# Optimization experiments

Hardware: AMD Instinct MI355X
Metric: run time of the kernel (lower is better)

## Reference

```python
import jax, jax.numpy as jnp
import numpy as np

N_NODES = 50000
N_EDGES = 800000
IN_FEATS = 128
HIDDEN = 128
OUT_LEN = 128


def setup_inputs() -> dict:
    key = jax.random.key(0)
    ks = jax.random.split(key, 8)
    feat = jax.random.normal(ks[0], (N_NODES, IN_FEATS), dtype=jnp.float32)
    # Glorot-ish init for weights, zeros for bias (DGL GraphConv default)
    def w(k, fi, fo):
        return jax.random.normal(k, (fi, fo), dtype=jnp.float32) / np.sqrt(fi)
    W1 = w(ks[1], IN_FEATS, HIDDEN)
    W2 = w(ks[2], HIDDEN, HIDDEN)
    W3 = w(ks[3], HIDDEN, OUT_LEN)
    b1 = jnp.zeros((HIDDEN,), jnp.float32)
    b2 = jnp.zeros((HIDDEN,), jnp.float32)
    b3 = jnp.zeros((OUT_LEN,), jnp.float32)
    src = jax.random.randint(ks[4], (N_EDGES,), 0, N_NODES, dtype=jnp.int32)
    dst = jax.random.randint(ks[5], (N_EDGES,), 0, N_NODES, dtype=jnp.int32)
    return {"feat": feat, "W1": W1, "b1": b1, "W2": W2, "b2": b2,
            "W3": W3, "b3": b3, "src": src, "dst": dst}


def _degree_norm(idx, n):
    # degree counts, clamped to min 1 (DGL behavior), then ^{-1/2}
    deg = jax.ops.segment_sum(jnp.ones_like(idx, dtype=jnp.float32), idx,
                              num_segments=n)
    return jax.lax.rsqrt(jnp.maximum(deg, 1.0))


def _graph_conv(x, W, b, src, dst, out_norm, in_norm):
    # DGL GraphConv, norm='both':
    # h = D_dst^{-1/2} * segsum_dst( D_src^{-1/2} * x[src] ) @ W + b
    h = x * out_norm[:, None]
    m = jax.ops.segment_sum(h[src], dst, num_segments=x.shape[0])  # [N, d]
    m = m * in_norm[:, None]
    return m @ W + b


def reference(feat, W1, b1, W2, b2, W3, b3, src, dst):
    out_norm = _degree_norm(src, feat.shape[0])  # out-degree norm (source)
    in_norm = _degree_norm(dst, feat.shape[0])   # in-degree norm (dest)
    h = jax.nn.relu(_graph_conv(feat, W1, b1, src, dst, out_norm, in_norm))
    h = jax.nn.relu(_graph_conv(h, W2, b2, src, dst, out_norm, in_norm))
    h = _graph_conv(h, W3, b3, src, dst, out_norm, in_norm)
    # single graph: mean_nodes == mean over all nodes, then squeeze -> [out_len]
    return jnp.mean(h, axis=0)
```

## Files before the change

kernel.cpp:

```cpp
#include <hip/hip_runtime.h>

#define N_NODES 50000
#define N_EDGES 800000
#define F 128
#define SCAN_NB 49
#define CH 64
#define EPC (N_EDGES / CH)
#define HALF 25000
#define QTR 12500
#define BSTRIDE 17
#define AGG_NB (N_NODES / 4)
#define RED_NB 256

typedef __bf16 bf16x8 __attribute__((ext_vector_type(8)));
typedef float  f32x4  __attribute__((ext_vector_type(4)));
typedef float  f32x2  __attribute__((ext_vector_type(2)));

__device__ inline unsigned short f2bf(float f) {
    unsigned u = __float_as_uint(f);
    u += 0x7FFF + ((u >> 16) & 1);
    return (unsigned short)(u >> 16);
}
__device__ inline unsigned packbf2(float a, float b) {
    return (unsigned)f2bf(a) | ((unsigned)f2bf(b) << 16);
}

__device__ inline void fp8x8_to_f32(uint2 u, float* f) {
    f32x2 v0 = __builtin_amdgcn_cvt_pk_f32_fp8(u.x, false);
    f32x2 v1 = __builtin_amdgcn_cvt_pk_f32_fp8(u.x, true);
    f32x2 v2 = __builtin_amdgcn_cvt_pk_f32_fp8(u.y, false);
    f32x2 v3 = __builtin_amdgcn_cvt_pk_f32_fp8(u.y, true);
    f[0] = v0.x; f[1] = v0.y; f[2] = v1.x; f[3] = v1.y;
    f[4] = v2.x; f[5] = v2.y; f[6] = v3.x; f[7] = v3.y;
}
__device__ inline unsigned f32x4_to_fp8(float a, float b, float c, float d) {
    unsigned r = __builtin_amdgcn_cvt_pk_fp8_f32(a, b, 0, false);
    r = __builtin_amdgcn_cvt_pk_fp8_f32(c, d, r, true);
    return r;
}

__global__ __launch_bounds__(1024) void hist_kernel(const int* __restrict__ src,
                                                    const int* __restrict__ dst,
                                                    int* __restrict__ Hs,
                                                    int* __restrict__ Hd) {
    __shared__ unsigned hist[HALF / 2];
    int bx = blockIdx.x;
    int c = bx >> 2, t = bx & 1, h = (bx >> 1) & 1;
    const int* ids = t ? dst : src;
    int* H = t ? Hd : Hs;
    int base = h * HALF;
    for (int j = threadIdx.x; j < HALF / 2; j += 1024) hist[j] = 0;
    __syncthreads();
    int e0 = c * EPC;
    for (int e = e0 + threadIdx.x; e < e0 + EPC; e += 1024) {
        int id = ids[e] - base;
        if ((unsigned)id < (unsigned)HALF)
            atomicAdd(&hist[id >> 1], 1u << ((id & 1) * 16));
    }
    __syncthreads();
    for (int j = threadIdx.x; j < HALF / 2; j += 1024) {
        unsigned u = hist[j];
        uint2 o; o.x = u & 0xFFFFu; o.y = u >> 16;
        *(uint2*)&H[(size_t)c * N_NODES + base + 2 * j] = o;
    }
}

__global__ __launch_bounds__(1024) void reduceN_kernel(const int* __restrict__ Hs,
                                                       const int* __restrict__ Hd,
                                                       float* __restrict__ onorm,
                                                       float* __restrict__ inorm,
                                                       int* __restrict__ degd,
                                                       int* __restrict__ bsums) {
    __shared__ int wsum[16];
    int i = blockIdx.x * 1024 + threadIdx.x;
    int dd = 0;
    if (i < N_NODES) {
        int ds = 0;
        for (int c = 0; c < CH; c++) {
            ds += Hs[(size_t)c * N_NODES + i];
            dd += Hd[(size_t)c * N_NODES + i];
        }
        onorm[i] = rsqrtf(fmaxf((float)ds, 1.0f));
        inorm[i] = rsqrtf(fmaxf((float)dd, 1.0f));
        degd[i] = dd;
    }
    int v = dd;
#pragma unroll
    for (int off = 32; off; off >>= 1) v += __shfl_down(v, off);
    if ((threadIdx.x & 63) == 0) wsum[threadIdx.x >> 6] = v;
    __syncthreads();
    if (threadIdx.x == 0) {
        int s = 0;
#pragma unroll
        for (int k = 0; k < 16; k++) s += wsum[k];
        bsums[blockIdx.x] = s;
    }
}

__global__ __launch_bounds__(64) void scanB_kernel(const int* __restrict__ blockSums,
                                                   int* __restrict__ blockOffs) {
    int t = threadIdx.x;
    int v = (t < SCAN_NB) ? blockSums[t] : 0;
    int incl = v;
#pragma unroll
    for (int off = 1; off < 64; off <<= 1) {
        int u = __shfl_up(incl, off);
        if (t >= off) incl += u;
    }
    if (t < SCAN_NB) blockOffs[t] = incl - v;
}

__global__ __launch_bounds__(1024) void scanC_kernel(const int* __restrict__ deg,
                                                     const int* __restrict__ blockOffs,
                                                     int* __restrict__ rowst,
                                                     int* __restrict__ Hd) {
    __shared__ int wsum[16];
    int t = threadIdx.x, lane = t & 63, w = t >> 6;
    int i = blockIdx.x * 1024 + t;
    int v = (i < N_NODES) ? deg[i] : 0;
    int incl = v;
#pragma unroll
    for (int off = 1; off < 64; off <<= 1) {
        int u = __shfl_up(incl, off);
        if (lane >= off) incl += u;
    }
    if (lane == 63) wsum[w] = incl;
    __syncthreads();
    if (t == 0) {
        int s = 0;
#pragma unroll
        for (int k = 0; k < 16; k++) { int x = wsum[k]; wsum[k] = s; s += x; }
    }
    __syncthreads();
    incl += wsum[w] + blockOffs[blockIdx.x];
    if (i < N_NODES) {
        int s = incl - v;
        rowst[i] = s;
        if (i == N_NODES - 1) rowst[N_NODES] = incl;
        for (int c = 0; c < CH; c++) {
            size_t o = (size_t)c * N_NODES + i;
            int x = Hd[o]; Hd[o] = s; s += x;
        }
    }
}

__global__ __launch_bounds__(1024) void scatter2_kernel(const int* __restrict__ src,
                                                        const int* __restrict__ dst,
                                                        const float* __restrict__ onorm,
                                                        const int* __restrict__ P,
                                                        int2* __restrict__ epack) {
    __shared__ int cur[QTR];
    int bx = blockIdx.x;
    int c = bx >> 2, q = bx & 3;
    int base = q * QTR;
    for (int j = threadIdx.x; j < QTR; j += 1024)
        cur[j] = P[(size_t)c * N_NODES + base + j];
    __syncthreads();
    int e0 = c * EPC;
    for (int e = e0 + threadIdx.x; e < e0 + EPC; e += 1024) {
        int d = dst[e] - base;
        if ((unsigned)d < (unsigned)QTR) {
            int s = src[e];
            int pos = atomicAdd(&cur[d], 1);
            int2 p; p.x = s; p.y = __float_as_int(onorm[s]);
            epack[pos] = p;
        }
    }
}

__global__ __launch_bounds__(256) void cvt_kernel(const float* __restrict__ x,
                                                  uint2* __restrict__ xq, int n8) {
    int i = blockIdx.x * 256 + threadIdx.x;
    if (i < n8) {
        const float4* xv = (const float4*)x;
        float4 v0 = xv[i * 2], v1 = xv[i * 2 + 1];
        uint2 o;
        o.x = f32x4_to_fp8(v0.x, v0.y, v0.z, v0.w);
        o.y = f32x4_to_fp8(v1.x, v1.y, v1.z, v1.w);
        xq[i] = o;
    }
}

__global__ __launch_bounds__(128) void wprep_kernel(const float* __restrict__ W1,
                                                    const float* __restrict__ W2,
                                                    unsigned short* __restrict__ Wt_hi,
                                                    unsigned short* __restrict__ Wt_lo) {
    int bx = blockIdx.x;
    int wi = bx >> 7, n = bx & 127;
    const float* W = wi ? W2 : W1;
    int k = threadIdx.x;
    float v = W[k * F + n];
    unsigned short hi = f2bf(v);
    float r = v - __uint_as_float((unsigned)hi << 16);
    size_t o = (size_t)wi * F * F + (size_t)n * F + k;
    Wt_hi[o] = hi;
    Wt_lo[o] = f2bf(r);
}

template <int L3>
__global__ __launch_bounds__(256) void agg_csr_kernel(const uint2* __restrict__ xq,
                                                      uint4* __restrict__ mb,
                                                      float* __restrict__ part,
                                                      const int* __restrict__ rowst,
                                                      const int2* __restrict__ epack,
                                                      const float* __restrict__ inorm) {
    __shared__ float sP[4][F];
    int w = threadIdx.x >> 6;
    int lane = threadIdx.x & 63;
    int g = lane >> 4, t = lane & 15;
    int row = blockIdx.x * 4 + w;
    int beg = __builtin_amdgcn_readfirstlane(rowst[row]);
    int end = __builtin_amdgcn_readfirstlane(rowst[row + 1]);
    float acc[8];
#pragma unroll
    for (int k = 0; k < 8; k++) acc[k] = 0.0f;

    for (int e = beg; e < end; e += 16) {
        int ea = min(e + g,      end - 1);
        int eb = min(e + 4 + g,  end - 1);
        int ec = min(e + 8 + g,  end - 1);
        int ed = min(e + 12 + g, end - 1);
        int2 pa = epack[ea], pb = epack[eb], pc = epack[ec], pd = epack[ed];
        uint2 ua = xq[(size_t)pa.x * 16 + t];
        uint2 ub = xq[(size_t)pb.x * 16 + t];
        uint2 uc = xq[(size_t)pc.x * 16 + t];
        uint2 ud = xq[(size_t)pd.x * 16 + t];
        float wa = (e + g      < end) ? __int_as_float(pa.y) : 0.0f;
        float wb = (e + 4 + g  < end) ? __int_as_float(pb.y) : 0.0f;
        float wc = (e + 8 + g  < end) ? __int_as_float(pc.y) : 0.0f;
        float wd = (e + 12 + g < end) ? __int_as_float(pd.y) : 0.0f;
        float fa[8], fb[8], fc[8], fd[8];
        fp8x8_to_f32(ua, fa); fp8x8_to_f32(ub, fb);
        fp8x8_to_f32(uc, fc); fp8x8_to_f32(ud, fd);
#pragma unroll
        for (int k = 0; k < 8; k++)
            acc[k] += fa[k] * wa + fb[k] * wb + fc[k] * wc + fd[k] * wd;
    }
#pragma unroll
    for (int k = 0; k < 8; k++) {
        acc[k] += __shfl_xor(acc[k], 16, 64);
        acc[k] += __shfl_xor(acc[k], 32, 64);
    }
    float inw = inorm[row];
    if (!L3) {
        if (g == 0) {
            uint4 o;
            o.x = packbf2(acc[0] * inw, acc[1] * inw);
            o.y = packbf2(acc[2] * inw, acc[3] * inw);
            o.z = packbf2(acc[4] * inw, acc[5] * inw);
            o.w = packbf2(acc[6] * inw, acc[7] * inw);
            mb[(size_t)row * 16 + t] = o;
        }
    } else {
        if (g == 0) {
#pragma unroll
            for (int k = 0; k < 8; k++) sP[w][t * 8 + k] = acc[k] * inw;
        }
        __syncthreads();
        int tid = threadIdx.x;
        if (tid < F)
            part[(size_t)blockIdx.x * F + tid] =
                sP[0][tid] + sP[1][tid] + sP[2][tid] + sP[3][tid];
    }
}

__global__ __launch_bounds__(256) void mfma_gemm_kernel(const unsigned short* __restrict__ A,
                                                        const unsigned short* __restrict__ Wt_hi,
                                                        const unsigned short* __restrict__ Wt_lo,
                                                        const float* __restrict__ bias,
                                                        unsigned char* __restrict__ Y8) {
    __shared__ uint4 sB[F * BSTRIDE];
    int tid = threadIdx.x;
    int w = tid >> 6;
    int lane = tid & 63;
    int quad = lane >> 4, r16 = lane & 15;
    int row0 = blockIdx.x * 64 + w * 16;

    const uint4* Arow = (const uint4*)(A + (size_t)(row0 + r16) * F);
    uint4 a[4];
#pragma unroll
    for (int kk = 0; kk < 4; kk++) a[kk] = Arow[kk * 4 + quad];

    f32x4 acc[8];
#pragma unroll
    for (int t = 0; t < 8; t++) acc[t] = (f32x4){0.f, 0.f, 0.f, 0.f};

    const uint4* G[2] = {(const uint4*)Wt_hi, (const uint4*)Wt_lo};
#pragma unroll
    for (int ph = 0; ph < 2; ph++) {
        if (ph) __syncthreads();
        for (int j = tid; j < F * 16; j += 256)
            sB[(j >> 4) * BSTRIDE + (j & 15)] = G[ph][j];
        __syncthreads();
#pragma unroll
        for (int kk = 0; kk < 4; kk++) {
            bf16x8 av = __builtin_bit_cast(bf16x8, a[kk]);
#pragma unroll
            for (int t = 0; t < 8; t++) {
                bf16x8 bv = __builtin_bit_cast(bf16x8,
                    sB[(t * 16 + r16) * BSTRIDE + kk * 4 + quad]);
                acc[t] = __builtin_amdgcn_mfma_f32_16x16x32_bf16(av, bv, acc[t], 0, 0, 0);
            }
        }
    }

#pragma unroll
    for (int t = 0; t < 8; t++) {
        int col = t * 16 + r16;
        float bb = bias[col];
#pragma unroll
        for (int reg = 0; reg < 4; reg++) {
            int row = row0 + quad * 4 + reg;
            if (row < N_NODES) {
                float v = fmaxf(acc[t][reg] + bb, 0.0f);
                unsigned p = __builtin_amdgcn_cvt_pk_fp8_f32(v, v, 0, false);
                Y8[(size_t)row * F + col] = (unsigned char)(p & 0xFF);
            }
        }
    }
}

__global__ __launch_bounds__(128) void redpart_kernel(const float* __restrict__ part,
                                                      float* __restrict__ part2) {
    int tid = threadIdx.x;
    float acc = 0.0f;
    for (int r = blockIdx.x; r < AGG_NB; r += RED_NB)
        acc += part[(size_t)r * F + tid];
    part2[(size_t)blockIdx.x * F + tid] = acc;
}

__global__ __launch_bounds__(1024) void final_kernel(const float* __restrict__ part2,
                                                     const float* __restrict__ W3,
                                                     const float* __restrict__ b3,
                                                     float* __restrict__ out) {
    __shared__ float sc[8][F];
    int tid = threadIdx.x;
    int col = tid & 127, sl = tid >> 7;
    float acc = 0.0f;
    for (int b = sl; b < RED_NB; b += 8) acc += part2[(size_t)b * F + col];
    sc[sl][col] = acc;
    __syncthreads();
    if (tid < F) {
        float s = 0.0f;
#pragma unroll
        for (int k = 0; k < 8; k++) s += sc[k][tid];
        sc[0][tid] = s * (1.0f / (float)N_NODES);
    }
    __syncthreads();
    if (tid < F) {
        float o = b3[tid];
        for (int k = 0; k < F; k++) o += sc[0][k] * W3[k * F + tid];
        out[tid] = o;
    }
}

extern "C" void kernel_launch(void* const* d_in, const int* in_sizes, int n_in,
                              void* d_out, int out_size, void* d_ws, size_t ws_size,
                              hipStream_t stream) {
    const float* feat = (const float*)d_in[0];
    const float* W1   = (const float*)d_in[1];
    const float* b1   = (const float*)d_in[2];
    const float* W2   = (const float*)d_in[3];
    const float* b2   = (const float*)d_in[4];
    const float* W3   = (const float*)d_in[5];
    const float* b3   = (const float*)d_in[6];
    const int*   src  = (const int*)d_in[7];
    const int*   dst  = (const int*)d_in[8];
    float* out = (float*)d_out;

    char* ws = (char*)d_ws;
    size_t off = 0;
    int*   Hs    = (int*)  (ws + off);
    uint4* mb    = (uint4*)(ws + off); off += (size_t)CH * N_NODES * 4;
    int*   Hd    = (int*)  (ws + off);
    float* part  = (float*)(ws + off); off += (size_t)CH * N_NODES * 4;
    uint2* xq    = (uint2*)(ws + off); off += (size_t)N_NODES * F;
    uint2* hq    = (uint2*)(ws + off); off += (size_t)N_NODES * F;
    float* onorm = (float*)(ws + off); off += N_NODES * 4;
    float* inorm = (float*)(ws + off); off += N_NODES * 4;
    int*   rowst = (int*)  (ws + off); off += (N_NODES + 1) * 4;
    int*   bsums = (int*)  (ws + off); off += 64 * 4;
    int*   boffs = (int*)  (ws + off); off += 64 * 4;
    int*   degd  = (int*)  (ws + off); off += N_NODES * 4;
    unsigned short* Wt_hi = (unsigned short*)(ws + off); off += 2 * F * F * 2;
    unsigned short* Wt_lo = (unsigned short*)(ws + off); off += 2 * F * F * 2;
    float* part2 = (float*)(ws + off); off += (size_t)RED_NB * F * 4;
    int2*  epack = (int2*) (ws + off); off += (size_t)N_EDGES * 8;

    const int GB = (N_NODES + 63) / 64;

    hist_kernel<<<4 * CH, 1024, 0, stream>>>(src, dst, Hs, Hd);
    reduceN_kernel<<<SCAN_NB, 1024, 0, stream>>>(Hs, Hd, onorm, inorm, degd, bsums);
    scanB_kernel<<<1, 64, 0, stream>>>(bsums, boffs);
    scanC_kernel<<<SCAN_NB, 1024, 0, stream>>>(degd, boffs, rowst, Hd);
    scatter2_kernel<<<4 * CH, 1024, 0, stream>>>(src, dst, onorm, Hd, epack);

    cvt_kernel<<<(N_NODES * F / 8 + 255) / 256, 256, 0, stream>>>(feat, xq, N_NODES * F / 8);
    wprep_kernel<<<256, 128, 0, stream>>>(W1, W2, Wt_hi, Wt_lo);

    agg_csr_kernel<0><<<AGG_NB, 256, 0, stream>>>(xq, mb, part, rowst, epack, inorm);
    mfma_gemm_kernel<<<GB, 256, 0, stream>>>((const unsigned short*)mb, Wt_hi, Wt_lo, b1,
                                             (unsigned char*)hq);
    agg_csr_kernel<0><<<AGG_NB, 256, 0, stream>>>(hq, mb, part, rowst, epack, inorm);
    mfma_gemm_kernel<<<GB, 256, 0, stream>>>((const unsigned short*)mb, Wt_hi + F * F,
                                             Wt_lo + F * F, b2, (unsigned char*)xq);
    agg_csr_kernel<1><<<AGG_NB, 256, 0, stream>>>(xq, mb, part, rowst, epack, inorm);
    redpart_kernel<<<RED_NB, 128, 0, stream>>>(part, part2);
    final_kernel<<<1, 1024, 0, stream>>>(part2, W3, b3, out);
}
```

Measured before the change: 259.6 us.

## Replace third-layer aggregation with weighted column sum and fold source norm into features

The last layer's sum over destination nodes of the aggregated messages is rewritten algebraically: each source node's contribution is weighted by q[s] = sum of inorm[dst] over its out-edges, computed once by a new tq_kernel. That replaces the third full edge-gather aggregation with a single weighted column sum over nodes. The source out-degree norm is now applied when features are quantised (cvt and GEMM epilogue), so the edge list stores only 4-byte source ids instead of 8-byte id/weight pairs. Histograms move to 16-bit counts to cut workspace traffic. The cost is an extra atomic pass over the edges for q and changed rounding, since scaling now happens before fp8 quantisation.

Measured after the change: 245.9 us. 5.3% less time.

```diff
diff --git a/kernel.cpp b/kernel.cpp
--- a/kernel.cpp
+++ b/kernel.cpp
@@ -41,13 +41,13 @@
 
 __global__ __launch_bounds__(1024) void hist_kernel(const int* __restrict__ src,
                                                     const int* __restrict__ dst,
-                                                    int* __restrict__ Hs,
-                                                    int* __restrict__ Hd) {
+                                                    unsigned short* __restrict__ Hs16,
+                                                    unsigned short* __restrict__ Hd16) {
     __shared__ unsigned hist[HALF / 2];
     int bx = blockIdx.x;
     int c = bx >> 2, t = bx & 1, h = (bx >> 1) & 1;
     const int* ids = t ? dst : src;
-    int* H = t ? Hd : Hs;
+    unsigned short* H = t ? Hd16 : Hs16;
     int base = h * HALF;
     for (int j = threadIdx.x; j < HALF / 2; j += 1024) hist[j] = 0;
     __syncthreads();
@@ -58,15 +58,12 @@
             atomicAdd(&hist[id >> 1], 1u << ((id & 1) * 16));
     }
     __syncthreads();
-    for (int j = threadIdx.x; j < HALF / 2; j += 1024) {
-        unsigned u = hist[j];
-        uint2 o; o.x = u & 0xFFFFu; o.y = u >> 16;
-        *(uint2*)&H[(size_t)c * N_NODES + base + 2 * j] = o;
-    }
-}
-
-__global__ __launch_bounds__(1024) void reduceN_kernel(const int* __restrict__ Hs,
-                                                       const int* __restrict__ Hd,
+    for (int j = threadIdx.x; j < HALF / 2; j += 1024)
+        *(unsigned*)&H[(size_t)c * N_NODES + base + 2 * j] = hist[j];
+}
+
+__global__ __launch_bounds__(1024) void reduceN_kernel(const unsigned short* __restrict__ Hs16,
+                                                       const unsigned short* __restrict__ Hd16,
                                                        float* __restrict__ onorm,
                                                        float* __restrict__ inorm,
                                                        int* __restrict__ degd,
@@ -77,8 +74,8 @@
     if (i < N_NODES) {
         int ds = 0;
         for (int c = 0; c < CH; c++) {
-            ds += Hs[(size_t)c * N_NODES + i];
-            dd += Hd[(size_t)c * N_NODES + i];
+            ds += Hs16[(size_t)c * N_NODES + i];
+            dd += Hd16[(size_t)c * N_NODES + i];
         }
         onorm[i] = rsqrtf(fmaxf((float)ds, 1.0f));
         inorm[i] = rsqrtf(fmaxf((float)dd, 1.0f));
@@ -110,10 +107,34 @@
     if (t < SCAN_NB) blockOffs[t] = incl - v;
 }
 
+__global__ __launch_bounds__(1024) void tq_kernel(const int* __restrict__ src,
+                                                  const int* __restrict__ dst,
+                                                  const float* __restrict__ inorm,
+                                                  float* __restrict__ Tq) {
+    __shared__ float a[QTR];
+    int bx = blockIdx.x;
+    int c = bx >> 2, q = bx & 3;
+    int base = q * QTR;
+    for (int j = threadIdx.x; j < QTR; j += 1024) a[j] = 0.0f;
+    __syncthreads();
+    int e0 = c * EPC;
+    for (int e = e0 + threadIdx.x; e < e0 + EPC; e += 1024) {
+        int s = src[e] - base;
+        if ((unsigned)s < (unsigned)QTR)
+            atomicAdd(&a[s], inorm[dst[e]]);
+    }
+    __syncthreads();
+    for (int j = threadIdx.x; j < QTR; j += 1024)
+        Tq[(size_t)c * N_NODES + base + j] = a[j];
+}
+
 __global__ __launch_bounds__(1024) void scanC_kernel(const int* __restrict__ deg,
                                                      const int* __restrict__ blockOffs,
                                                      int* __restrict__ rowst,
-                                                     int* __restrict__ Hd) {
+                                                     const unsigned short* __restrict__ Hd16,
+                                                     int* __restrict__ P,
+                                                     const float* __restrict__ Tq,
+                                                     float* __restrict__ qt) {
     __shared__ int wsum[16];
     int t = threadIdx.x, lane = t & 63, w = t >> 6;
     int i = blockIdx.x * 1024 + t;
@@ -137,18 +158,20 @@
         int s = incl - v;
         rowst[i] = s;
         if (i == N_NODES - 1) rowst[N_NODES] = incl;
+        float tsum = 0.0f;
         for (int c = 0; c < CH; c++) {
             size_t o = (size_t)c * N_NODES + i;
-            int x = Hd[o]; Hd[o] = s; s += x;
+            P[o] = s; s += Hd16[o];
+            tsum += Tq[o];
         }
+        qt[i] = tsum;
     }
 }
 
 __global__ __launch_bounds__(1024) void scatter2_kernel(const int* __restrict__ src,
                                                         const int* __restrict__ dst,
-                                                        const float* __restrict__ onorm,
                                                         const int* __restrict__ P,
-                                                        int2* __restrict__ epack) {
+                                                        int* __restrict__ esrc) {
     __shared__ int cur[QTR];
     int bx = blockIdx.x;
     int c = bx >> 2, q = bx & 3;
@@ -160,23 +183,23 @@
     for (int e = e0 + threadIdx.x; e < e0 + EPC; e += 1024) {
         int d = dst[e] - base;
         if ((unsigned)d < (unsigned)QTR) {
-            int s = src[e];
             int pos = atomicAdd(&cur[d], 1);
-            int2 p; p.x = s; p.y = __float_as_int(onorm[s]);
-            epack[pos] = p;
+            esrc[pos] = src[e];
         }
     }
 }
 
 __global__ __launch_bounds__(256) void cvt_kernel(const float* __restrict__ x,
+                                                  const float* __restrict__ onorm,
                                                   uint2* __restrict__ xq, int n8) {
     int i = blockIdx.x * 256 + threadIdx.x;
     if (i < n8) {
+        float w = onorm[i >> 4];
         const float4* xv = (const float4*)x;
         float4 v0 = xv[i * 2], v1 = xv[i * 2 + 1];
         uint2 o;
-        o.x = f32x4_to_fp8(v0.x, v0.y, v0.z, v0.w);
-        o.y = f32x4_to_fp8(v1.x, v1.y, v1.z, v1.w);
+        o.x = f32x4_to_fp8(v0.x * w, v0.y * w, v0.z * w, v0.w * w);
+        o.y = f32x4_to_fp8(v1.x * w, v1.y * w, v1.z * w, v1.w * w);
         xq[i] = o;
     }
 }
@@ -197,14 +220,11 @@
     Wt_lo[o] = f2bf(r);
 }
 
-template <int L3>
 __global__ __launch_bounds__(256) void agg_csr_kernel(const uint2* __restrict__ xq,
                                                       uint4* __restrict__ mb,
-                                                      float* __restrict__ part,
                                                       const int* __restrict__ rowst,
-                                                      const int2* __restrict__ epack,
+                                                      const int* __restrict__ esrc,
                                                       const float* __restrict__ inorm) {
-    __shared__ float sP[4][F];
     int w = threadIdx.x >> 6;
     int lane = threadIdx.x & 63;
     int g = lane >> 4, t = lane & 15;
@@ -220,15 +240,15 @@
         int eb = min(e + 4 + g,  end - 1);
         int ec = min(e + 8 + g,  end - 1);
         int ed = min(e + 12 + g, end - 1);
-        int2 pa = epack[ea], pb = epack[eb], pc = epack[ec], pd = epack[ed];
-        uint2 ua = xq[(size_t)pa.x * 16 + t];
-        uint2 ub = xq[(size_t)pb.x * 16 + t];
-        uint2 uc = xq[(size_t)pc.x * 16 + t];
-        uint2 ud = xq[(size_t)pd.x * 16 + t];
-        float wa = (e + g      < end) ? __int_as_float(pa.y) : 0.0f;
-        float wb = (e + 4 + g  < end) ? __int_as_float(pb.y) : 0.0f;
-        float wc = (e + 8 + g  < end) ? __int_as_float(pc.y) : 0.0f;
-        float wd = (e + 12 + g < end) ? __int_as_float(pd.y) : 0.0f;
+        int sa = esrc[ea], sb = esrc[eb], sc = esrc[ec], sd = esrc[ed];
+        uint2 ua = xq[(size_t)sa * 16 + t];
+        uint2 ub = xq[(size_t)sb * 16 + t];
+        uint2 uc = xq[(size_t)sc * 16 + t];
+        uint2 ud = xq[(size_t)sd * 16 + t];
+        float wa = (e + g      < end) ? 1.0f : 0.0f;
+        float wb = (e + 4 + g  < end) ? 1.0f : 0.0f;
+        float wc = (e + 8 + g  < end) ? 1.0f : 0.0f;
+        float wd = (e + 12 + g < end) ? 1.0f : 0.0f;
         float fa[8], fb[8], fc[8], fd[8];
         fp8x8_to_f32(ua, fa); fp8x8_to_f32(ub, fb);
         fp8x8_to_f32(uc, fc); fp8x8_to_f32(ud, fd);
@@ -241,26 +261,14 @@
         acc[k] += __shfl_xor(acc[k], 16, 64);
         acc[k] += __shfl_xor(acc[k], 32, 64);
     }
-    float inw = inorm[row];
-    if (!L3) {
-        if (g == 0) {
-            uint4 o;
-            o.x = packbf2(acc[0] * inw, acc[1] * inw);
-            o.y = packbf2(acc[2] * inw, acc[3] * inw);
-            o.z = packbf2(acc[4] * inw, acc[5] * inw);
-            o.w = packbf2(acc[6] * inw, acc[7] * inw);
-            mb[(size_t)row * 16 + t] = o;
-        }
-    } else {
-        if (g == 0) {
-#pragma unroll
-            for (int k = 0; k < 8; k++) sP[w][t * 8 + k] = acc[k] * inw;
-        }
-        __syncthreads();
-        int tid = threadIdx.x;
-        if (tid < F)
-            part[(size_t)blockIdx.x * F + tid] =
-                sP[0][tid] + sP[1][tid] + sP[2][tid] + sP[3][tid];
+    if (g == 0) {
+        float inw = inorm[row];
+        uint4 o;
+        o.x = packbf2(acc[0] * inw, acc[1] * inw);
+        o.y = packbf2(acc[2] * inw, acc[3] * inw);
+        o.z = packbf2(acc[4] * inw, acc[5] * inw);
+        o.w = packbf2(acc[6] * inw, acc[7] * inw);
+        mb[(size_t)row * 16 + t] = o;
     }
 }
 
@@ -268,6 +276,7 @@
                                                         const unsigned short* __restrict__ Wt_hi,
                                                         const unsigned short* __restrict__ Wt_lo,
                                                         const float* __restrict__ bias,
+                                                        const float* __restrict__ onorm,
                                                         unsigned char* __restrict__ Y8) {
     __shared__ uint4 sB[F * BSTRIDE];
     int tid = threadIdx.x;
@@ -304,6 +313,12 @@
         }
     }
 
+    float onw[4];
+#pragma unroll
+    for (int reg = 0; reg < 4; reg++) {
+        int row = row0 + quad * 4 + reg;
+        onw[reg] = (row < N_NODES) ? onorm[row] : 0.0f;
+    }
 #pragma unroll
     for (int t = 0; t < 8; t++) {
         int col = t * 16 + r16;
@@ -312,7 +327,7 @@
         for (int reg = 0; reg < 4; reg++) {
             int row = row0 + quad * 4 + reg;
             if (row < N_NODES) {
-                float v = fmaxf(acc[t][reg] + bb, 0.0f);
+                float v = fmaxf(acc[t][reg] + bb, 0.0f) * onw[reg];
                 unsigned p = __builtin_amdgcn_cvt_pk_fp8_f32(v, v, 0, false);
                 Y8[(size_t)row * F + col] = (unsigned char)(p & 0xFF);
             }
@@ -320,13 +335,24 @@
     }
 }
 
-__global__ __launch_bounds__(128) void redpart_kernel(const float* __restrict__ part,
-                                                      float* __restrict__ part2) {
+__global__ __launch_bounds__(256) void colsum_kernel(const unsigned short* __restrict__ x8,
+                                                     const float* __restrict__ qt,
+                                                     float* __restrict__ part2) {
+    __shared__ float sP[4][F];
     int tid = threadIdx.x;
-    float acc = 0.0f;
-    for (int r = blockIdx.x; r < AGG_NB; r += RED_NB)
-        acc += part[(size_t)r * F + tid];
-    part2[(size_t)blockIdx.x * F + tid] = acc;
+    int w = tid >> 6, lane = tid & 63;
+    float a0 = 0.0f, a1 = 0.0f;
+    for (int r = blockIdx.x * 4 + w; r < N_NODES; r += RED_NB * 4) {
+        float q = qt[r];
+        unsigned us = x8[(size_t)r * 64 + lane];
+        f32x2 v = __builtin_amdgcn_cvt_pk_f32_fp8(us, false);
+        a0 += v.x * q; a1 += v.y * q;
+    }
+    sP[w][lane * 2] = a0; sP[w][lane * 2 + 1] = a1;
+    __syncthreads();
+    if (tid < F)
+        part2[(size_t)blockIdx.x * F + tid] =
+            sP[0][tid] + sP[1][tid] + sP[2][tid] + sP[3][tid];
 }
 
 __global__ __launch_bounds__(1024) void final_kernel(const float* __restrict__ part2,
@@ -370,41 +396,43 @@
 
     char* ws = (char*)d_ws;
     size_t off = 0;
-    int*   Hs    = (int*)  (ws + off);
-    uint4* mb    = (uint4*)(ws + off); off += (size_t)CH * N_NODES * 4;
-    int*   Hd    = (int*)  (ws + off);
-    float* part  = (float*)(ws + off); off += (size_t)CH * N_NODES * 4;
+    uint4* mb    = (uint4*)(ws + off); off += (size_t)N_NODES * F * 2;
+    float* Tq    = (float*)(ws + off); off += (size_t)CH * N_NODES * 4;
+    int*   P     = (int*)  (ws + off); off += (size_t)CH * N_NODES * 4;
+    unsigned short* Hs16 = (unsigned short*)(ws + off); off += (size_t)CH * N_NODES * 2;
+    unsigned short* Hd16 = (unsigned short*)(ws + off); off += (size_t)CH * N_NODES * 2;
     uint2* xq    = (uint2*)(ws + off); off += (size_t)N_NODES * F;
     uint2* hq    = (uint2*)(ws + off); off += (size_t)N_NODES * F;
+    unsigned short* Wt_hi = (unsigned short*)(ws + off); off += 2 * F * F * 2;
+    unsigned short* Wt_lo = (unsigned short*)(ws + off); off += 2 * F * F * 2;
+    float* part2 = (float*)(ws + off); off += (size_t)RED_NB * F * 4;
+    int*   esrc  = (int*)  (ws + off); off += (size_t)N_EDGES * 4;
     float* onorm = (float*)(ws + off); off += N_NODES * 4;
     float* inorm = (float*)(ws + off); off += N_NODES * 4;
+    float* qt    = (float*)(ws + off); off += N_NODES * 4;
+    int*   degd  = (int*)  (ws + off); off += N_NODES * 4;
     int*   rowst = (int*)  (ws + off); off += (N_NODES + 1) * 4;
     int*   bsums = (int*)  (ws + off); off += 64 * 4;
     int*   boffs = (int*)  (ws + off); off += 64 * 4;
-    int*   degd  = (int*)  (ws + off); off += N_NODES * 4;
-    unsigned short* Wt_hi = (unsigned short*)(ws + off); off += 2 * F * F * 2;
-    unsigned short* Wt_lo = (unsigned short*)(ws + off); off += 2 * F * F * 2;
-    float* part2 = (float*)(ws + off); off += (size_t)RED_NB * F * 4;
-    int2*  epack = (int2*) (ws + off); off += (size_t)N_EDGES * 8;
 
     const int GB = (N_NODES + 63) / 64;
 
-    hist_kernel<<<4 * CH, 1024, 0, stream>>>(src, dst, Hs, Hd);
-    reduceN_kernel<<<SCAN_NB, 1024, 0, stream>>>(Hs, Hd, onorm, inorm, degd, bsums);
+    hist_kernel<<<4 * CH, 1024, 0, stream>>>(src, dst, Hs16, Hd16);
+    reduceN_kernel<<<SCAN_NB, 1024, 0, stream>>>(Hs16, Hd16, onorm, inorm, degd, bsums);
     scanB_kernel<<<1, 64, 0, stream>>>(bsums, boffs);
-    scanC_kernel<<<SCAN_NB, 1024, 0, stream>>>(degd, boffs, rowst, Hd);
-    scatter2_kernel<<<4 * CH, 1024, 0, stream>>>(src, dst, onorm, Hd, epack);
-
-    cvt_kernel<<<(N_NODES * F / 8 + 255) / 256, 256, 0, stream>>>(feat, xq, N_NODES * F / 8);
+    tq_kernel<<<4 * CH, 1024, 0, stream>>>(src, dst, inorm, Tq);
+    scanC_kernel<<<SCAN_NB, 1024, 0, stream>>>(degd, boffs, rowst, Hd16, P, Tq, qt);
+    scatter2_kernel<<<4 * CH, 1024, 0, stream>>>(src, dst, P, esrc);
+
+    cvt_kernel<<<(N_NODES * F / 8 + 255) / 256, 256, 0, stream>>>(feat, onorm, xq, N_NODES * F / 8);
     wprep_kernel<<<256, 128, 0, stream>>>(W1, W2, Wt_hi, Wt_lo);
 
-    agg_csr_kernel<0><<<AGG_NB, 256, 0, stream>>>(xq, mb, part, rowst, epack, inorm);
+    agg_csr_kernel<<<AGG_NB, 256, 0, stream>>>(xq, mb, rowst, esrc, inorm);
     mfma_gemm_kernel<<<GB, 256, 0, stream>>>((const unsigned short*)mb, Wt_hi, Wt_lo, b1,
-                                             (unsigned char*)hq);
-    agg_csr_kernel<0><<<AGG_NB, 256, 0, stream>>>(hq, mb, part, rowst, epack, inorm);
+                                             onorm, (unsigned char*)hq);
+    agg_csr_kernel<<<AGG_NB, 256, 0, stream>>>(hq, mb, rowst, esrc, inorm);
     mfma_gemm_kernel<<<GB, 256, 0, stream>>>((const unsigned short*)mb, Wt_hi + F * F,
-                                             Wt_lo + F * F, b2, (unsigned char*)xq);
-    agg_csr_kernel<1><<<AGG_NB, 256, 0, stream>>>(xq, mb, part, rowst, epack, inorm);
-    redpart_kernel<<<RED_NB, 128, 0, stream>>>(part, part2);
+                                             Wt_lo + F * F, b2, onorm, (unsigned char*)xq);
+    colsum_kernel<<<RED_NB, 256, 0, stream>>>((const unsigned short*)xq, qt, part2);
     final_kernel<<<1, 1024, 0, stream>>>(part2, W3, b3, out);
 }
```
